# Kernel tuning notes

Measured on AMD Instinct MI355X. Metric: run time of the kernel, lower is better.

## Reference

```python
import jax, jax.numpy as jnp
import numpy as np

HID = 64  # GRU hidden size fixed in source: layers.GRU(64, ...)


def setup_inputs() -> dict:
    key = jax.random.key(0)
    ks = jax.random.split(key, 9)
    B, T, D, K = 128, 1024, 128, 32
    s = 0.05
    X = jax.random.normal(ks[0], (B, T, D), jnp.float32)
    mask = jnp.ones((B, T), jnp.int32)  # 1 = valid token
    # Keras GRU (reset_after=True) params
    gru_kernel = jax.random.normal(ks[1], (D, 3 * HID), jnp.float32) * s
    gru_rec_kernel = jax.random.normal(ks[2], (HID, 3 * HID), jnp.float32) * s
    gru_bias = jax.random.normal(ks[3], (2, 3 * HID), jnp.float32) * s  # [input_bias, recurrent_bias]
    # tfa.layers.CRF params: dense projection + chain kernel + boundary energies
    dense_kernel = jax.random.normal(ks[4], (HID, K), jnp.float32) * s
    dense_bias = jax.random.normal(ks[5], (K,), jnp.float32) * s
    chain_kernel = jax.random.normal(ks[6], (K, K), jnp.float32) * s
    left_boundary = jax.random.normal(ks[7], (K,), jnp.float32) * s
    right_boundary = jax.random.normal(ks[8], (K,), jnp.float32) * s
    return {"X": X, "mask": mask, "gru_kernel": gru_kernel,
            "gru_rec_kernel": gru_rec_kernel, "gru_bias": gru_bias,
            "dense_kernel": dense_kernel, "dense_bias": dense_bias,
            "chain_kernel": chain_kernel, "left_boundary": left_boundary,
            "right_boundary": right_boundary}


def gru_forward(X, mask_bool, gru_kernel, gru_rec_kernel, gru_bias):
    # Keras GRU, reset_after=True: z/r/h gate ordering, tanh/sigmoid activations.
    B, T, D = X.shape
    xproj = X @ gru_kernel + gru_bias[0]  # [B,T,3H] input projection (fused GEMM)

    def step(h, inp):
        xp, mt = inp  # xp: [B,3H], mt: [B] bool
        rec = h @ gru_rec_kernel + gru_bias[1]  # [B,3H]
        xz, xr, xh = jnp.split(xp, 3, axis=-1)
        rz, rr, rh = jnp.split(rec, 3, axis=-1)
        z = jax.nn.sigmoid(xz + rz)
        r = jax.nn.sigmoid(xr + rr)
        hh = jnp.tanh(xh + r * rh)
        hn = z * h + (1.0 - z) * hh
        hn = jnp.where(mt[:, None], hn, h)  # masked steps carry state
        return hn, hn

    h0 = jnp.zeros((B, HID), X.dtype)
    _, hs = jax.lax.scan(step, h0, (jnp.swapaxes(xproj, 0, 1), jnp.swapaxes(mask_bool, 0, 1)))
    return jnp.swapaxes(hs, 0, 1)  # [B,T,H]


def viterbi_decode(potentials, chain_kernel):
    # Max-plus DP with backpointers; potentials: [B,T,K]
    pots = jnp.swapaxes(potentials, 0, 1)  # [T,B,K]

    def fwd(score, pot_t):
        s = score[:, :, None] + chain_kernel[None]  # [B,K_from,K_to]
        bp = jnp.argmax(s, axis=1).astype(jnp.int32)  # [B,K]
        new_score = jnp.max(s, axis=1) + pot_t
        return new_score, bp

    final_score, bps = jax.lax.scan(fwd, pots[0], pots[1:])  # bps: [T-1,B,K]
    last_tag = jnp.argmax(final_score, axis=-1).astype(jnp.int32)  # [B]

    def back(tag, bp):
        prev = jnp.take_along_axis(bp, tag[:, None], axis=1)[:, 0]
        return prev, tag

    first_tag, tags = jax.lax.scan(back, last_tag, bps, reverse=True)  # tags[t] = tag at step t+1
    decoded = jnp.concatenate([first_tag[None], tags], axis=0)  # [T,B]
    return jnp.swapaxes(decoded, 0, 1)  # [B,T]


def reference(X, mask, gru_kernel, gru_rec_kernel, gru_bias,
              dense_kernel, dense_bias, chain_kernel,
              left_boundary, right_boundary):
    B, T, D = X.shape
    mask_bool = mask == 1
    hidden = gru_forward(X, mask_bool, gru_kernel, gru_rec_kernel, gru_bias)
    potentials = hidden @ dense_kernel + dense_bias  # [B,T,K] emissions
    seq_len = jnp.sum(mask, axis=1).astype(jnp.int32)  # [B]
    # Boundary energies (tfa CRF use_boundary=True): left at t=0, right at last valid step
    potentials = potentials.at[:, 0].add(left_boundary)
    potentials = potentials.at[jnp.arange(B), seq_len - 1].add(right_boundary)
    decoded = viterbi_decode(potentials, chain_kernel)  # [B,T] int32
    return decoded, potentials, seq_len, chain_kernel
```

## Files before the change

### kernel.cpp

```cpp
#include <hip/hip_runtime.h>
#include <math.h>

#define BB 128
#define TT 1024
#define DD 128
#define HH 64
#define G3 192
#define KK 32
#define CH 32

__global__ __launch_bounds__(256, 2) void xproj_kernel(const float* __restrict__ X,
                                                       const float* __restrict__ Wk,
                                                       const float* __restrict__ gbias,
                                                       float* __restrict__ xp) {
    __shared__ float Xs[64 * 132];
    __shared__ float Ws[128 * 68];
    const int tid = threadIdx.x;
    const int row0 = blockIdx.x * 64;
    const int cg = blockIdx.y;
#pragma unroll
    for (int it = 0; it < 8; ++it) {
        int idx = it * 1024 + tid * 4;
        int r = idx >> 7, c = idx & 127;
        float4 v = *(const float4*)&X[((size_t)(row0 + r)) * DD + c];
        *(float4*)&Xs[r * 132 + c] = v;
    }
#pragma unroll
    for (int it = 0; it < 8; ++it) {
        int idx = it * 1024 + tid * 4;
        int k = idx >> 6, c = idx & 63;
        float4 v = *(const float4*)&Wk[(size_t)k * G3 + cg * 64 + c];
        *(float4*)&Ws[k * 68 + c] = v;
    }
    __syncthreads();
    const int tr = tid >> 4, tc = tid & 15;
    const int r0 = tr * 4, c0 = tc * 4;
    float acc[4][4];
#pragma unroll
    for (int r = 0; r < 4; ++r)
#pragma unroll
        for (int c = 0; c < 4; ++c) acc[r][c] = 0.f;
#pragma unroll 4
    for (int k = 0; k < DD; k += 4) {
        float a[4][4];
#pragma unroll
        for (int r = 0; r < 4; ++r) {
            float4 t = *(const float4*)&Xs[(r0 + r) * 132 + k];
            a[r][0] = t.x; a[r][1] = t.y; a[r][2] = t.z; a[r][3] = t.w;
        }
#pragma unroll
        for (int kk = 0; kk < 4; ++kk) {
            float4 b = *(const float4*)&Ws[(k + kk) * 68 + c0];
#pragma unroll
            for (int r = 0; r < 4; ++r) {
                acc[r][0] += a[r][kk] * b.x;
                acc[r][1] += a[r][kk] * b.y;
                acc[r][2] += a[r][kk] * b.z;
                acc[r][3] += a[r][kk] * b.w;
            }
        }
    }
    float4 bias = *(const float4*)&gbias[cg * 64 + c0];
#pragma unroll
    for (int r = 0; r < 4; ++r) {
        float4 o;
        o.x = acc[r][0] + bias.x; o.y = acc[r][1] + bias.y;
        o.z = acc[r][2] + bias.z; o.w = acc[r][3] + bias.w;
        *(float4*)&xp[((size_t)(row0 + r0 + r)) * G3 + cg * 64 + c0] = o;
    }
}

#define BCAST(v, l) __int_as_float(__builtin_amdgcn_readlane(__float_as_int(v), (l)))

__global__ __launch_bounds__(320, 1)
void fused_kernel(const float* __restrict__ xp,
                  const float* __restrict__ Wr,
                  const float* __restrict__ gbias,
                  const int* __restrict__ mask,
                  const float* __restrict__ Dk,
                  const float* __restrict__ db,
                  const float* __restrict__ chain,
                  const float* __restrict__ lb,
                  const float* __restrict__ rb,
                  float* __restrict__ out_pot,
                  float* __restrict__ out_dec,
                  float* __restrict__ out_slen,
                  float* __restrict__ out_chn) {
    const int b = blockIdx.x;
    const int tid = threadIdx.x;
    const int w = tid >> 6;
    const int l = tid & 63;
    const int bTT = b * TT;

    __shared__ unsigned char bp[(TT - 1) * KK];
    __shared__ unsigned char table[32 * 32 * KK];
    __shared__ int ent[32];
    __shared__ int last_tag_s;
    __shared__ float gbuf[2][4 * HH];
    __shared__ __align__(16) float hbuf[4][HH];
    __shared__ __align__(16) float potring[64][KK];
    __shared__ __align__(16) float xpstage[2][CH * G3];
    __shared__ int maskst[2][CH];

    if (w < 3) {
        const int j = l;
        float wg[HH];
#pragma unroll
        for (int i2 = 0; i2 < HH; ++i2) wg[i2] = Wr[i2 * G3 + w * HH + j];
#pragma unroll
        for (int i2 = 0; i2 < HH; ++i2) asm volatile("" : "+v"(wg[i2]));
        const float bw = gbias[G3 + w * HH + j];
        __builtin_amdgcn_s_setprio(1);
        float h = 0.f;
        __syncthreads();
        float xv0 = xpstage[0][tid];
        int m0 = maskst[0][0];
        for (int i = 0; i < TT + 2; ++i) {
            if (i < TT) {
                float a0 = bw, a1 = 0.f, a2 = 0.f, a3 = 0.f;
#pragma unroll
                for (int c = 0; c < HH; c += 4) {
                    a0 += BCAST(h, c + 0) * wg[c + 0];
                    a1 += BCAST(h, c + 1) * wg[c + 1];
                    a2 += BCAST(h, c + 2) * wg[c + 2];
                    a3 += BCAST(h, c + 3) * wg[c + 3];
                }
                float a = (a0 + a1) + (a2 + a3);
                float g = (w == 2) ? a : 1.f / (1.f + __expf(-(xv0 + a)));
                gbuf[i & 1][w * HH + j] = g;
                if (w == 2) gbuf[i & 1][3 * HH + j] = xv0;
            }
            __syncthreads();
            if (i < TT) {
                float z  = gbuf[i & 1][j];
                float r  = gbuf[i & 1][HH + j];
                float rh = gbuf[i & 1][2 * HH + j];
                float xh = gbuf[i & 1][3 * HH + j];
                float y = xh + r * rh;
                float hh = 1.f - 2.f / (1.f + __expf(2.f * y));
                float hn = z * h + (1.f - z) * hh;
                hn = (m0 != 0) ? hn : h;
                h = hn;
                if (w == 0) hbuf[i & 3][j] = hn;
                if (i < TT - 1) {
                    const int t1 = i + 1;
                    xv0 = xpstage[(t1 >> 5) & 1][(t1 & 31) * G3 + tid];
                    m0  = maskst[(t1 >> 5) & 1][t1 & 31];
                }
            }
        }
    } else if (w == 3) {
        const int k = l & 31;
        int sl = 0;
#pragma unroll
        for (int q = 0; q < 16; ++q) sl += mask[bTT + q * 64 + l];
#pragma unroll
        for (int d = 32; d >= 1; d >>= 1) sl += __shfl_xor(sl, d, 64);
        if (l == 0) out_slen[b] = (float)sl;
        float dk[HH];
#pragma unroll
        for (int i2 = 0; i2 < HH; ++i2) dk[i2] = Dk[i2 * KK + k];
#pragma unroll
        for (int i2 = 0; i2 < HH; ++i2) asm volatile("" : "+v"(dk[i2]));
        const float dbk = db[k], lbk = lb[k], rbk = rb[k];
        const float* xpg = xp + (size_t)bTT * G3;
        float* potg = out_pot + (size_t)bTT * KK;
#pragma unroll
        for (int q = 0; q < 24; ++q) {
            float4 v = *(const float4*)&xpg[q * 256 + l * 4];
            *(float4*)&xpstage[0][q * 256 + l * 4] = v;
        }
        if (l < CH) maskst[0][l] = mask[bTT + l];
        __syncthreads();
        for (int i = 0; i < TT + 2; ++i) {
            if ((i & 31) == 0) {
                const int cn = (i >> 5) + 1;
                if (cn < 32) {
                    const float* src = xpg + (size_t)cn * CH * G3;
                    float* dst = &xpstage[cn & 1][0];
#pragma unroll
                    for (int q = 0; q < 24; ++q) {
                        float4 v = *(const float4*)&src[q * 256 + l * 4];
                        *(float4*)&dst[q * 256 + l * 4] = v;
                    }
                    if (l < CH) maskst[cn & 1][l] = mask[bTT + cn * CH + l];
                }
                const int cf = (i >> 5) - 2;
                if (cf >= 0) {
                    const float* srcl = &potring[(cf & 1) * 32][0];
                    float* dstg = potg + (size_t)cf * CH * KK;
#pragma unroll
                    for (int q = 0; q < 4; ++q) {
                        float4 v = *(const float4*)&srcl[q * 256 + l * 4];
                        *(float4*)&dstg[q * 256 + l * 4] = v;
                    }
                }
            }
            const int t = i - 2;
            if (t >= 0 && t < TT) {
                const float4* hv4 = (const float4*)&hbuf[t & 3][0];
                float p0 = dbk, p1 = 0.f, p2 = 0.f, p3 = 0.f;
#pragma unroll
                for (int c = 0; c < 16; ++c) {
                    float4 hv = hv4[c];
                    p0 += hv.x * dk[4 * c + 0];
                    p1 += hv.y * dk[4 * c + 1];
                    p2 += hv.z * dk[4 * c + 2];
                    p3 += hv.w * dk[4 * c + 3];
                }
                float pot = (p0 + p1) + (p2 + p3);
                if (t == 0) pot += lbk;
                if (t == sl - 1) pot += rbk;
                if (l < 32) potring[t & 63][k] = pot;
            }
            __syncthreads();
        }
        {
            const float* srcl = &potring[(31 & 1) * 32][0];
            float* dstg = potg + (size_t)31 * CH * KK;
#pragma unroll
            for (int q = 0; q < 4; ++q) {
                float4 v = *(const float4*)&srcl[q * 256 + l * 4];
                *(float4*)&dstg[q * 256 + l * 4] = v;
            }
        }
    } else {
        const int k = l & 31;
        const int hf = l >> 5;
        float ccol[16];
        int addr[16];
#pragma unroll
        for (int m = 0; m < 16; ++m) {
            ccol[m] = chain[(hf * 16 + m) * KK + k];
            addr[m] = (hf * 16 + m) * 4;
        }
#pragma unroll
        for (int m = 0; m < 16; ++m) asm volatile("" : "+v"(ccol[m]));
        const int addrx = (l ^ 32) * 4;
        float s = 0.f;
        __syncthreads();
        for (int i = 0; i < TT + 2; ++i) {
            __syncthreads();
            const int t = i - 2;
            if (t >= 0 && t < TT) {
                float pot = potring[t & 63][k];
                if (t == 0) {
                    s = pot;
                } else {
                    const int si = __float_as_int(s);
                    float c[16];
#pragma unroll
                    for (int m = 0; m < 16; ++m)
                        c[m] = __int_as_float(__builtin_amdgcn_ds_bpermute(addr[m], si)) + ccol[m];
                    float v1[8]; int i1[8];
#pragma unroll
                    for (int p = 0; p < 8; ++p) {
                        bool tk = c[2 * p + 1] > c[2 * p];
                        v1[p] = tk ? c[2 * p + 1] : c[2 * p];
                        i1[p] = hf * 16 + (tk ? 2 * p + 1 : 2 * p);
                    }
                    float v2[4]; int i2[4];
#pragma unroll
                    for (int p = 0; p < 4; ++p) {
                        bool tk = v1[2 * p + 1] > v1[2 * p];
                        v2[p] = tk ? v1[2 * p + 1] : v1[2 * p];
                        i2[p] = tk ? i1[2 * p + 1] : i1[2 * p];
                    }
                    float v3[2]; int i3[2];
#pragma unroll
                    for (int p = 0; p < 2; ++p) {
                        bool tk = v2[2 * p + 1] > v2[2 * p];
                        v3[p] = tk ? v2[2 * p + 1] : v2[2 * p];
                        i3[p] = tk ? i2[2 * p + 1] : i2[2 * p];
                    }
                    bool tk = v3[1] > v3[0];
                    float bv = tk ? v3[1] : v3[0];
                    int bi = tk ? i3[1] : i3[0];
                    float ov = __int_as_float(__builtin_amdgcn_ds_bpermute(addrx, __float_as_int(bv)));
                    int   oi = __builtin_amdgcn_ds_bpermute(addrx, bi);
                    bool take = (ov > bv) || (ov == bv && oi < bi);
                    if (take) { bv = ov; bi = oi; }
                    if (l < 32) bp[(t - 1) * KK + k] = (unsigned char)bi;
                    s = bv + pot;
                }
            }
        }
        float bv = s; int bi = k;
#pragma unroll
        for (int d = 16; d >= 1; d >>= 1) {
            float ov = __shfl_xor(bv, d, 64);
            int   oi = __shfl_xor(bi, d, 64);
            bool take = (ov > bv) || (ov == bv && oi < bi);
            if (take) { bv = ov; bi = oi; }
        }
        if (l == 0) last_tag_s = bi;
    }
    __syncthreads();
    {
        const int k = tid & 31;
        const int grp = tid >> 5;
        for (int c = grp; c < 32; c += 10) {
            int tag = k;
            for (int ll = 31; ll >= 0; --ll) {
                const int t = c * 32 + ll;
                if (t < TT - 1) tag = bp[t * KK + tag];
                table[(c * 32 + ll) * KK + k] = (unsigned char)tag;
            }
        }
    }
    __syncthreads();
    if (tid == 0) {
        int e = last_tag_s;
        ent[31] = e;
        for (int c = 30; c >= 0; --c) { e = table[(c + 1) * 32 * KK + e]; ent[c] = e; }
    }
    __syncthreads();
    for (int t = tid; t < TT; t += 320) {
        const int c = t >> 5, ll = t & 31;
        out_dec[(size_t)bTT + t] = (float)table[(c * 32 + ll) * KK + ent[c]];
    }
    if (b == 0) {
        for (int i2 = tid; i2 < KK * KK; i2 += 320) out_chn[i2] = chain[i2];
    }
}

extern "C" void kernel_launch(void* const* d_in, const int* in_sizes, int n_in,
                              void* d_out, int out_size, void* d_ws, size_t ws_size,
                              hipStream_t stream) {
    const float* X     = (const float*)d_in[0];
    const int*   mask  = (const int*)d_in[1];
    const float* Wk    = (const float*)d_in[2];
    const float* Wr    = (const float*)d_in[3];
    const float* gb    = (const float*)d_in[4];
    const float* Dk    = (const float*)d_in[5];
    const float* db    = (const float*)d_in[6];
    const float* chain = (const float*)d_in[7];
    const float* lb    = (const float*)d_in[8];
    const float* rb    = (const float*)d_in[9];

    float* out = (float*)d_out;
    float* out_dec  = out;
    float* out_pot  = out + (size_t)BB * TT;
    float* out_slen = out + (size_t)BB * TT + (size_t)BB * TT * KK;
    float* out_chn  = out_slen + BB;

    float* xp = (float*)d_ws;

    xproj_kernel<<<dim3((BB * TT) / 64, 3), dim3(256), 0, stream>>>(X, Wk, gb, xp);
    fused_kernel<<<dim3(BB), dim3(320), 0, stream>>>(xp, Wr, gb, mask, Dk, db, chain,
                                                     lb, rb, out_pot, out_dec,
                                                     out_slen, out_chn);
}
```

Measured before the change: 898.2 us.

## Fuse GRU input projection into the recurrent kernel via producer warps

Drops the separate input-projection GEMM kernel and its workspace round trip. Three new wavefronts in the fused kernel compute the xproj chunks on the fly: each keeps a column of the input weights in registers and stages X through the backtrace table buffer, which is reused as scratch. The work is pipelined one chunk ahead of the recurrence with a per-step barrier. This removes a kernel launch and the global write and read of the projections, but raises the block to 512 threads and adds per-step work that the serial recurrence may have to wait on.

```diff
diff --git a/kernel.cpp b/kernel.cpp
--- a/kernel.cpp
+++ b/kernel.cpp
@@ -9,71 +9,11 @@
 #define KK 32
 #define CH 32
 
-__global__ __launch_bounds__(256, 2) void xproj_kernel(const float* __restrict__ X,
-                                                       const float* __restrict__ Wk,
-                                                       const float* __restrict__ gbias,
-                                                       float* __restrict__ xp) {
-    __shared__ float Xs[64 * 132];
-    __shared__ float Ws[128 * 68];
-    const int tid = threadIdx.x;
-    const int row0 = blockIdx.x * 64;
-    const int cg = blockIdx.y;
-#pragma unroll
-    for (int it = 0; it < 8; ++it) {
-        int idx = it * 1024 + tid * 4;
-        int r = idx >> 7, c = idx & 127;
-        float4 v = *(const float4*)&X[((size_t)(row0 + r)) * DD + c];
-        *(float4*)&Xs[r * 132 + c] = v;
-    }
-#pragma unroll
-    for (int it = 0; it < 8; ++it) {
-        int idx = it * 1024 + tid * 4;
-        int k = idx >> 6, c = idx & 63;
-        float4 v = *(const float4*)&Wk[(size_t)k * G3 + cg * 64 + c];
-        *(float4*)&Ws[k * 68 + c] = v;
-    }
-    __syncthreads();
-    const int tr = tid >> 4, tc = tid & 15;
-    const int r0 = tr * 4, c0 = tc * 4;
-    float acc[4][4];
-#pragma unroll
-    for (int r = 0; r < 4; ++r)
-#pragma unroll
-        for (int c = 0; c < 4; ++c) acc[r][c] = 0.f;
-#pragma unroll 4
-    for (int k = 0; k < DD; k += 4) {
-        float a[4][4];
-#pragma unroll
-        for (int r = 0; r < 4; ++r) {
-            float4 t = *(const float4*)&Xs[(r0 + r) * 132 + k];
-            a[r][0] = t.x; a[r][1] = t.y; a[r][2] = t.z; a[r][3] = t.w;
-        }
-#pragma unroll
-        for (int kk = 0; kk < 4; ++kk) {
-            float4 b = *(const float4*)&Ws[(k + kk) * 68 + c0];
-#pragma unroll
-            for (int r = 0; r < 4; ++r) {
-                acc[r][0] += a[r][kk] * b.x;
-                acc[r][1] += a[r][kk] * b.y;
-                acc[r][2] += a[r][kk] * b.z;
-                acc[r][3] += a[r][kk] * b.w;
-            }
-        }
-    }
-    float4 bias = *(const float4*)&gbias[cg * 64 + c0];
-#pragma unroll
-    for (int r = 0; r < 4; ++r) {
-        float4 o;
-        o.x = acc[r][0] + bias.x; o.y = acc[r][1] + bias.y;
-        o.z = acc[r][2] + bias.z; o.w = acc[r][3] + bias.w;
-        *(float4*)&xp[((size_t)(row0 + r0 + r)) * G3 + cg * 64 + c0] = o;
-    }
-}
-
 #define BCAST(v, l) __int_as_float(__builtin_amdgcn_readlane(__float_as_int(v), (l)))
 
-__global__ __launch_bounds__(320, 1)
-void fused_kernel(const float* __restrict__ xp,
+__global__ __launch_bounds__(512, 1)
+void fused_kernel(const float* __restrict__ X,
+                  const float* __restrict__ Wk,
                   const float* __restrict__ Wr,
                   const float* __restrict__ gbias,
                   const int* __restrict__ mask,
@@ -93,7 +33,7 @@
     const int bTT = b * TT;
 
     __shared__ unsigned char bp[(TT - 1) * KK];
-    __shared__ unsigned char table[32 * 32 * KK];
+    __shared__ __align__(16) unsigned char table[32 * 32 * KK];
     __shared__ int ent[32];
     __shared__ int last_tag_s;
     __shared__ float gbuf[2][4 * HH];
@@ -102,6 +42,9 @@
     __shared__ __align__(16) float xpstage[2][CH * G3];
     __shared__ int maskst[2][CH];
 
+    float* Xstage0 = (float*)&table[0];
+    float* Xstage1 = (float*)&table[CH * DD * 4];
+
     if (w < 3) {
         const int j = l;
         float wg[HH];
@@ -112,6 +55,7 @@
         const float bw = gbias[G3 + w * HH + j];
         __builtin_amdgcn_s_setprio(1);
         float h = 0.f;
+        __syncthreads();
         __syncthreads();
         float xv0 = xpstage[0][tid];
         int m0 = maskst[0][0];
@@ -163,28 +107,14 @@
 #pragma unroll
         for (int i2 = 0; i2 < HH; ++i2) asm volatile("" : "+v"(dk[i2]));
         const float dbk = db[k], lbk = lb[k], rbk = rb[k];
-        const float* xpg = xp + (size_t)bTT * G3;
         float* potg = out_pot + (size_t)bTT * KK;
-#pragma unroll
-        for (int q = 0; q < 24; ++q) {
-            float4 v = *(const float4*)&xpg[q * 256 + l * 4];
-            *(float4*)&xpstage[0][q * 256 + l * 4] = v;
-        }
         if (l < CH) maskst[0][l] = mask[bTT + l];
+        __syncthreads();
         __syncthreads();
         for (int i = 0; i < TT + 2; ++i) {
             if ((i & 31) == 0) {
                 const int cn = (i >> 5) + 1;
-                if (cn < 32) {
-                    const float* src = xpg + (size_t)cn * CH * G3;
-                    float* dst = &xpstage[cn & 1][0];
-#pragma unroll
-                    for (int q = 0; q < 24; ++q) {
-                        float4 v = *(const float4*)&src[q * 256 + l * 4];
-                        *(float4*)&dst[q * 256 + l * 4] = v;
-                    }
-                    if (l < CH) maskst[cn & 1][l] = mask[bTT + cn * CH + l];
-                }
+                if (cn < 32 && l < CH) maskst[cn & 1][l] = mask[bTT + cn * CH + l];
                 const int cf = (i >> 5) - 2;
                 if (cf >= 0) {
                     const float* srcl = &potring[(cf & 1) * 32][0];
@@ -224,6 +154,81 @@
                 *(float4*)&dstg[q * 256 + l * 4] = v;
             }
         }
+    } else if (w < 7) {
+        const int xw = w - 4;
+        const int col = xw * 64 + l;
+        float wk[DD];
+#pragma unroll
+        for (int k2 = 0; k2 < DD; ++k2) wk[k2] = Wk[(size_t)k2 * G3 + col];
+#pragma unroll
+        for (int k2 = 0; k2 < DD; ++k2) asm volatile("" : "+v"(wk[k2]));
+        const float b0 = gbias[col];
+        const float* Xg = X + (size_t)bTT * DD;
+        {
+            const float* src0 = Xg;
+            const float* src1 = Xg + (size_t)CH * DD;
+#pragma unroll
+            for (int q = 0; q < 6; ++q) {
+                int idx = q * 192 + col;
+                if (idx < 1024) {
+                    float4 v0 = *(const float4*)&src0[idx * 4];
+                    *(float4*)&Xstage0[idx * 4] = v0;
+                    float4 v1 = *(const float4*)&src1[idx * 4];
+                    *(float4*)&Xstage1[idx * 4] = v1;
+                }
+            }
+        }
+        __syncthreads();
+#pragma unroll 1
+        for (int r = 0; r < CH; ++r) {
+            const float4* xr = (const float4*)&Xstage0[r * DD];
+            float acc = 0.f;
+#pragma unroll 4
+            for (int c4 = 0; c4 < 32; ++c4) {
+                float4 xv = xr[c4];
+                acc += xv.x * wk[4 * c4 + 0];
+                acc += xv.y * wk[4 * c4 + 1];
+                acc += xv.z * wk[4 * c4 + 2];
+                acc += xv.w * wk[4 * c4 + 3];
+            }
+            xpstage[0][r * G3 + col] = acc + b0;
+        }
+        __syncthreads();
+        for (int i = 0; i < TT + 2; ++i) {
+            const int wi = i >> 5;
+            if ((i & 31) == 0) {
+                const int cs = wi + 2;
+                if (cs < 32) {
+                    const float* src = Xg + (size_t)cs * CH * DD;
+                    float* dst = (cs & 1) ? Xstage1 : Xstage0;
+#pragma unroll
+                    for (int q = 0; q < 6; ++q) {
+                        int idx = q * 192 + col;
+                        if (idx < 1024) {
+                            float4 v = *(const float4*)&src[idx * 4];
+                            *(float4*)&dst[idx * 4] = v;
+                        }
+                    }
+                }
+            }
+            const int c = wi + 1;
+            if (c < 32) {
+                const int r = i & 31;
+                const float* xsrc = (c & 1) ? Xstage1 : Xstage0;
+                const float4* xr = (const float4*)&xsrc[r * DD];
+                float acc = 0.f;
+#pragma unroll 4
+                for (int c4 = 0; c4 < 32; ++c4) {
+                    float4 xv = xr[c4];
+                    acc += xv.x * wk[4 * c4 + 0];
+                    acc += xv.y * wk[4 * c4 + 1];
+                    acc += xv.z * wk[4 * c4 + 2];
+                    acc += xv.w * wk[4 * c4 + 3];
+                }
+                xpstage[c & 1][r * G3 + col] = acc + b0;
+            }
+            __syncthreads();
+        }
     } else {
         const int k = l & 31;
         const int hf = l >> 5;
@@ -238,6 +243,7 @@
         for (int m = 0; m < 16; ++m) asm volatile("" : "+v"(ccol[m]));
         const int addrx = (l ^ 32) * 4;
         float s = 0.f;
+        __syncthreads();
         __syncthreads();
         for (int i = 0; i < TT + 2; ++i) {
             __syncthreads();
@@ -299,7 +305,7 @@
     {
         const int k = tid & 31;
         const int grp = tid >> 5;
-        for (int c = grp; c < 32; c += 10) {
+        for (int c = grp; c < 32; c += 16) {
             int tag = k;
             for (int ll = 31; ll >= 0; --ll) {
                 const int t = c * 32 + ll;
@@ -315,12 +321,12 @@
         for (int c = 30; c >= 0; --c) { e = table[(c + 1) * 32 * KK + e]; ent[c] = e; }
     }
     __syncthreads();
-    for (int t = tid; t < TT; t += 320) {
+    for (int t = tid; t < TT; t += 512) {
         const int c = t >> 5, ll = t & 31;
         out_dec[(size_t)bTT + t] = (float)table[(c * 32 + ll) * KK + ent[c]];
     }
     if (b == 0) {
-        for (int i2 = tid; i2 < KK * KK; i2 += 320) out_chn[i2] = chain[i2];
+        for (int i2 = tid; i2 < KK * KK; i2 += 512) out_chn[i2] = chain[i2];
     }
 }
 
@@ -344,10 +350,7 @@
     float* out_slen = out + (size_t)BB * TT + (size_t)BB * TT * KK;
     float* out_chn  = out_slen + BB;
 
-    float* xp = (float*)d_ws;
-
-    xproj_kernel<<<dim3((BB * TT) / 64, 3), dim3(256), 0, stream>>>(X, Wk, gb, xp);
-    fused_kernel<<<dim3(BB), dim3(320), 0, stream>>>(xp, Wr, gb, mask, Dk, db, chain,
-                                                     lb, rb, out_pot, out_dec,
+    fused_kernel<<<dim3(BB), dim3(512), 0, stream>>>(X, Wk, Wr, gb, mask, Dk, db,
+                                                     chain, lb, rb, out_pot, out_dec,
                                                      out_slen, out_chn);
 }
```

After: 3.111 ms. 246% more time.

## Merge input projection and recurrent kernel into one launch with per-chunk flag handoff

Applied to the files above, without the earlier changes.

Replaces the separate projection GEMM launch with a single kernel of 2*BB blocks. The first BB blocks compute each sequence's input projection in 64-row tiles and raise global flags as tiles finish. The remaining BB blocks run the GRU/CRF recurrence and spin on those flags before staging each chunk, so the projection overlaps the serial recurrence instead of running before it. The cost is one block per sequence doing the GEMM, which is less parallel than the old grid, and the scheme depends on producer blocks being co-resident with the spinning consumers to avoid deadlock.

```diff
diff --git a/kernel.cpp b/kernel.cpp
--- a/kernel.cpp
+++ b/kernel.cpp
@@ -9,98 +9,112 @@
 #define KK 32
 #define CH 32
 
-__global__ __launch_bounds__(256, 2) void xproj_kernel(const float* __restrict__ X,
-                                                       const float* __restrict__ Wk,
-                                                       const float* __restrict__ gbias,
-                                                       float* __restrict__ xp) {
-    __shared__ float Xs[64 * 132];
-    __shared__ float Ws[128 * 68];
+#define BCAST(v, l) __int_as_float(__builtin_amdgcn_readlane(__float_as_int(v), (l)))
+
+__device__ int g_flags[BB * 32];
+
+__global__ __launch_bounds__(320, 1)
+void mega_kernel(const float* __restrict__ X,
+                 const float* __restrict__ Wk,
+                 const float* __restrict__ Wr,
+                 const float* __restrict__ gbias,
+                 const int* __restrict__ mask,
+                 const float* __restrict__ Dk,
+                 const float* __restrict__ db,
+                 const float* __restrict__ chain,
+                 const float* __restrict__ lb,
+                 const float* __restrict__ rb,
+                 float* __restrict__ xp,
+                 float* __restrict__ out_pot,
+                 float* __restrict__ out_dec,
+                 float* __restrict__ out_slen,
+                 float* __restrict__ out_chn) {
+    __shared__ __align__(16) unsigned char smem[138240];
     const int tid = threadIdx.x;
-    const int row0 = blockIdx.x * 64;
-    const int cg = blockIdx.y;
-#pragma unroll
-    for (int it = 0; it < 8; ++it) {
-        int idx = it * 1024 + tid * 4;
-        int r = idx >> 7, c = idx & 127;
-        float4 v = *(const float4*)&X[((size_t)(row0 + r)) * DD + c];
-        *(float4*)&Xs[r * 132 + c] = v;
-    }
-#pragma unroll
-    for (int it = 0; it < 8; ++it) {
-        int idx = it * 1024 + tid * 4;
-        int k = idx >> 6, c = idx & 63;
-        float4 v = *(const float4*)&Wk[(size_t)k * G3 + cg * 64 + c];
-        *(float4*)&Ws[k * 68 + c] = v;
-    }
-    __syncthreads();
-    const int tr = tid >> 4, tc = tid & 15;
-    const int r0 = tr * 4, c0 = tc * 4;
-    float acc[4][4];
-#pragma unroll
-    for (int r = 0; r < 4; ++r)
-#pragma unroll
-        for (int c = 0; c < 4; ++c) acc[r][c] = 0.f;
+
+    if (blockIdx.x < BB) {
+        const int p = blockIdx.x;
+        const int bTT = p * TT;
+        float* Xs = (float*)smem;
+        float* Ws = (float*)(smem + 33792);
+        for (int idx = tid; idx < 6144; idx += 320) {
+            const int cg = idx >> 11, rem = idx & 2047;
+            const int k = rem >> 4, c4 = (rem & 15) << 2;
+            float4 v = *(const float4*)&Wk[(size_t)k * G3 + cg * 64 + c4];
+            *(float4*)&Ws[cg * (128 * 68) + k * 68 + c4] = v;
+        }
+        const int tr = tid >> 4, tc = tid & 15;
+        const int r0 = tr * 4, c0 = tc * 4;
+        for (int rt = 0; rt < 16; ++rt) {
+            const int row0 = rt * 64;
+            for (int idx = tid; idx < 2048; idx += 320) {
+                const int r = idx >> 5, c4 = (idx & 31) << 2;
+                float4 v = *(const float4*)&X[((size_t)(bTT + row0 + r)) * DD + c4];
+                *(float4*)&Xs[r * 132 + c4] = v;
+            }
+            __syncthreads();
+            if (tid < 256) {
+                for (int cg = 0; cg < 3; ++cg) {
+                    const float* Wc = &Ws[cg * (128 * 68)];
+                    float acc[4][4];
+#pragma unroll
+                    for (int r = 0; r < 4; ++r)
+#pragma unroll
+                        for (int c = 0; c < 4; ++c) acc[r][c] = 0.f;
 #pragma unroll 4
-    for (int k = 0; k < DD; k += 4) {
-        float a[4][4];
-#pragma unroll
-        for (int r = 0; r < 4; ++r) {
-            float4 t = *(const float4*)&Xs[(r0 + r) * 132 + k];
-            a[r][0] = t.x; a[r][1] = t.y; a[r][2] = t.z; a[r][3] = t.w;
-        }
-#pragma unroll
-        for (int kk = 0; kk < 4; ++kk) {
-            float4 b = *(const float4*)&Ws[(k + kk) * 68 + c0];
-#pragma unroll
-            for (int r = 0; r < 4; ++r) {
-                acc[r][0] += a[r][kk] * b.x;
-                acc[r][1] += a[r][kk] * b.y;
-                acc[r][2] += a[r][kk] * b.z;
-                acc[r][3] += a[r][kk] * b.w;
-            }
-        }
-    }
-    float4 bias = *(const float4*)&gbias[cg * 64 + c0];
-#pragma unroll
-    for (int r = 0; r < 4; ++r) {
-        float4 o;
-        o.x = acc[r][0] + bias.x; o.y = acc[r][1] + bias.y;
-        o.z = acc[r][2] + bias.z; o.w = acc[r][3] + bias.w;
-        *(float4*)&xp[((size_t)(row0 + r0 + r)) * G3 + cg * 64 + c0] = o;
-    }
-}
-
-#define BCAST(v, l) __int_as_float(__builtin_amdgcn_readlane(__float_as_int(v), (l)))
-
-__global__ __launch_bounds__(320, 1)
-void fused_kernel(const float* __restrict__ xp,
-                  const float* __restrict__ Wr,
-                  const float* __restrict__ gbias,
-                  const int* __restrict__ mask,
-                  const float* __restrict__ Dk,
-                  const float* __restrict__ db,
-                  const float* __restrict__ chain,
-                  const float* __restrict__ lb,
-                  const float* __restrict__ rb,
-                  float* __restrict__ out_pot,
-                  float* __restrict__ out_dec,
-                  float* __restrict__ out_slen,
-                  float* __restrict__ out_chn) {
-    const int b = blockIdx.x;
-    const int tid = threadIdx.x;
+                    for (int k = 0; k < DD; k += 4) {
+                        float a[4][4];
+#pragma unroll
+                        for (int r = 0; r < 4; ++r) {
+                            float4 t = *(const float4*)&Xs[(r0 + r) * 132 + k];
+                            a[r][0] = t.x; a[r][1] = t.y; a[r][2] = t.z; a[r][3] = t.w;
+                        }
+#pragma unroll
+                        for (int kk = 0; kk < 4; ++kk) {
+                            float4 bv = *(const float4*)&Wc[(k + kk) * 68 + c0];
+#pragma unroll
+                            for (int r = 0; r < 4; ++r) {
+                                acc[r][0] += a[r][kk] * bv.x;
+                                acc[r][1] += a[r][kk] * bv.y;
+                                acc[r][2] += a[r][kk] * bv.z;
+                                acc[r][3] += a[r][kk] * bv.w;
+                            }
+                        }
+                    }
+                    float4 bias = *(const float4*)&gbias[cg * 64 + c0];
+#pragma unroll
+                    for (int r = 0; r < 4; ++r) {
+                        float4 o;
+                        o.x = acc[r][0] + bias.x; o.y = acc[r][1] + bias.y;
+                        o.z = acc[r][2] + bias.z; o.w = acc[r][3] + bias.w;
+                        *(float4*)&xp[((size_t)(bTT + row0 + r0 + r)) * G3 + cg * 64 + c0] = o;
+                    }
+                }
+            }
+            __threadfence();
+            __syncthreads();
+            if (tid == 0) {
+                atomicExch(&g_flags[p * 32 + 2 * rt], 1);
+                atomicExch(&g_flags[p * 32 + 2 * rt + 1], 1);
+            }
+        }
+        return;
+    }
+
+    const int b = blockIdx.x - BB;
     const int w = tid >> 6;
     const int l = tid & 63;
     const int bTT = b * TT;
 
-    __shared__ unsigned char bp[(TT - 1) * KK];
-    __shared__ unsigned char table[32 * 32 * KK];
-    __shared__ int ent[32];
-    __shared__ int last_tag_s;
-    __shared__ float gbuf[2][4 * HH];
-    __shared__ __align__(16) float hbuf[4][HH];
-    __shared__ __align__(16) float potring[64][KK];
-    __shared__ __align__(16) float xpstage[2][CH * G3];
-    __shared__ int maskst[2][CH];
+    unsigned char* bp    = smem;
+    unsigned char* table = smem + 32736;
+    int*   ent        = (int*)(smem + 65504);
+    int*   last_tag_s = (int*)(smem + 65632);
+    float (*gbuf)[4 * HH]   = (float (*)[4 * HH])(smem + 65648);
+    float (*hbuf)[HH]       = (float (*)[HH])(smem + 67696);
+    float (*potring)[KK]    = (float (*)[KK])(smem + 68720);
+    float (*xpstage)[CH * G3] = (float (*)[CH * G3])(smem + 76912);
+    int (*maskst)[CH]       = (int (*)[CH])(smem + 126064);
 
     if (w < 3) {
         const int j = l;
@@ -165,6 +179,10 @@
         const float dbk = db[k], lbk = lb[k], rbk = rb[k];
         const float* xpg = xp + (size_t)bTT * G3;
         float* potg = out_pot + (size_t)bTT * KK;
+        if (l == 0) {
+            while (atomicAdd(&g_flags[b * 32], 0) == 0) __builtin_amdgcn_s_sleep(8);
+        }
+        __threadfence();
 #pragma unroll
         for (int q = 0; q < 24; ++q) {
             float4 v = *(const float4*)&xpg[q * 256 + l * 4];
@@ -176,6 +194,11 @@
             if ((i & 31) == 0) {
                 const int cn = (i >> 5) + 1;
                 if (cn < 32) {
+                    if (l == 0) {
+                        while (atomicAdd(&g_flags[b * 32 + cn], 0) == 0)
+                            __builtin_amdgcn_s_sleep(8);
+                    }
+                    __threadfence();
                     const float* src = xpg + (size_t)cn * CH * G3;
                     float* dst = &xpstage[cn & 1][0];
 #pragma unroll
@@ -293,7 +316,7 @@
             bool take = (ov > bv) || (ov == bv && oi < bi);
             if (take) { bv = ov; bi = oi; }
         }
-        if (l == 0) last_tag_s = bi;
+        if (l == 0) *last_tag_s = bi;
     }
     __syncthreads();
     {
@@ -310,7 +333,7 @@
     }
     __syncthreads();
     if (tid == 0) {
-        int e = last_tag_s;
+        int e = *last_tag_s;
         ent[31] = e;
         for (int c = 30; c >= 0; --c) { e = table[(c + 1) * 32 * KK + e]; ent[c] = e; }
     }
@@ -319,9 +342,10 @@
         const int c = t >> 5, ll = t & 31;
         out_dec[(size_t)bTT + t] = (float)table[(c * 32 + ll) * KK + ent[c]];
     }
-    if (b == 0) {
+    if (blockIdx.x == BB) {
         for (int i2 = tid; i2 < KK * KK; i2 += 320) out_chn[i2] = chain[i2];
     }
+    for (int i2 = tid; i2 < 32; i2 += 320) atomicExch(&g_flags[b * 32 + i2], 0);
 }
 
 extern "C" void kernel_launch(void* const* d_in, const int* in_sizes, int n_in,
@@ -346,8 +370,7 @@
 
     float* xp = (float*)d_ws;
 
-    xproj_kernel<<<dim3((BB * TT) / 64, 3), dim3(256), 0, stream>>>(X, Wk, gb, xp);
-    fused_kernel<<<dim3(BB), dim3(320), 0, stream>>>(xp, Wr, gb, mask, Dk, db, chain,
-                                                     lb, rb, out_pot, out_dec,
-                                                     out_slen, out_chn);
+    mega_kernel<<<dim3(2 * BB), dim3(320), 0, stream>>>(X, Wk, Wr, gb, mask, Dk, db,
+                                                        chain, lb, rb, xp, out_pot,
+                                                        out_dec, out_slen, out_chn);
 }
```

Measured after the change: 926.0 us. 1.03x slower.

## Split GRU and Viterbi into separate blocks linked by global flags

Applied to the files above, without the earlier changes.

The recurrence now runs in a single wave per batch row: that wave computes all three gates plus the emission projection, holding the z weights and dense kernel in registers and reading the r/h weights from LDS, so the per-step block-wide barrier disappears. Viterbi moves to a second set of blocks that poll per-chunk global flags and stream potentials from global memory into a double buffer in LDS. The aim is to shorten the serial per-timestep critical path by removing the cross-wave syncs. The cost is more work per step in one wave, extra LDS weight loads, and reliance on producer and consumer blocks being co-resident, which risks deadlock if the Viterbi blocks are scheduled before their GRU blocks.

```diff
diff --git a/kernel.cpp b/kernel.cpp
--- a/kernel.cpp
+++ b/kernel.cpp
@@ -8,6 +8,10 @@
 #define G3 192
 #define KK 32
 #define CH 32
+
+#define BCAST(v, l) __int_as_float(__builtin_amdgcn_readlane(__float_as_int(v), (l)))
+
+__device__ int g_pflags[BB * 32];
 
 __global__ __launch_bounds__(256, 2) void xproj_kernel(const float* __restrict__ X,
                                                        const float* __restrict__ Wk,
@@ -70,165 +74,141 @@
     }
 }
 
-#define BCAST(v, l) __int_as_float(__builtin_amdgcn_readlane(__float_as_int(v), (l)))
-
-__global__ __launch_bounds__(320, 1)
-void fused_kernel(const float* __restrict__ xp,
-                  const float* __restrict__ Wr,
-                  const float* __restrict__ gbias,
-                  const int* __restrict__ mask,
-                  const float* __restrict__ Dk,
-                  const float* __restrict__ db,
-                  const float* __restrict__ chain,
-                  const float* __restrict__ lb,
-                  const float* __restrict__ rb,
-                  float* __restrict__ out_pot,
-                  float* __restrict__ out_dec,
-                  float* __restrict__ out_slen,
-                  float* __restrict__ out_chn) {
-    const int b = blockIdx.x;
+__global__ __launch_bounds__(256, 1)
+void gruvit_kernel(const float* __restrict__ xp,
+                   const float* __restrict__ Wr,
+                   const float* __restrict__ gbias,
+                   const int* __restrict__ mask,
+                   const float* __restrict__ Dk,
+                   const float* __restrict__ db,
+                   const float* __restrict__ chain,
+                   const float* __restrict__ lb,
+                   const float* __restrict__ rb,
+                   float* __restrict__ out_pot,
+                   float* __restrict__ out_dec,
+                   float* __restrict__ out_slen,
+                   float* __restrict__ out_chn) {
     const int tid = threadIdx.x;
     const int w = tid >> 6;
     const int l = tid & 63;
-    const int bTT = b * TT;
-
+
+    __shared__ __align__(16) float wl[2][16][64][4];
     __shared__ unsigned char bp[(TT - 1) * KK];
-    __shared__ unsigned char table[32 * 32 * KK];
+    __shared__ __align__(16) unsigned char table[32 * 32 * KK];
+    __shared__ __align__(16) float potbuf[2][CH][KK];
     __shared__ int ent[32];
     __shared__ int last_tag_s;
-    __shared__ float gbuf[2][4 * HH];
-    __shared__ __align__(16) float hbuf[4][HH];
-    __shared__ __align__(16) float potring[64][KK];
-    __shared__ __align__(16) float xpstage[2][CH * G3];
-    __shared__ int maskst[2][CH];
-
-    if (w < 3) {
+
+    if (blockIdx.x < BB) {
+        if (w != 0) return;
+        const int b = blockIdx.x;
+        const int bTT = b * TT;
         const int j = l;
-        float wg[HH];
-#pragma unroll
-        for (int i2 = 0; i2 < HH; ++i2) wg[i2] = Wr[i2 * G3 + w * HH + j];
-#pragma unroll
-        for (int i2 = 0; i2 < HH; ++i2) asm volatile("" : "+v"(wg[i2]));
-        const float bw = gbias[G3 + w * HH + j];
-        __builtin_amdgcn_s_setprio(1);
-        float h = 0.f;
-        __syncthreads();
-        float xv0 = xpstage[0][tid];
-        int m0 = maskst[0][0];
-        for (int i = 0; i < TT + 2; ++i) {
-            if (i < TT) {
-                float a0 = bw, a1 = 0.f, a2 = 0.f, a3 = 0.f;
-#pragma unroll
-                for (int c = 0; c < HH; c += 4) {
-                    a0 += BCAST(h, c + 0) * wg[c + 0];
-                    a1 += BCAST(h, c + 1) * wg[c + 1];
-                    a2 += BCAST(h, c + 2) * wg[c + 2];
-                    a3 += BCAST(h, c + 3) * wg[c + 3];
-                }
-                float a = (a0 + a1) + (a2 + a3);
-                float g = (w == 2) ? a : 1.f / (1.f + __expf(-(xv0 + a)));
-                gbuf[i & 1][w * HH + j] = g;
-                if (w == 2) gbuf[i & 1][3 * HH + j] = xv0;
-            }
-            __syncthreads();
-            if (i < TT) {
-                float z  = gbuf[i & 1][j];
-                float r  = gbuf[i & 1][HH + j];
-                float rh = gbuf[i & 1][2 * HH + j];
-                float xh = gbuf[i & 1][3 * HH + j];
-                float y = xh + r * rh;
-                float hh = 1.f - 2.f / (1.f + __expf(2.f * y));
-                float hn = z * h + (1.f - z) * hh;
-                hn = (m0 != 0) ? hn : h;
-                h = hn;
-                if (w == 0) hbuf[i & 3][j] = hn;
-                if (i < TT - 1) {
-                    const int t1 = i + 1;
-                    xv0 = xpstage[(t1 >> 5) & 1][(t1 & 31) * G3 + tid];
-                    m0  = maskst[(t1 >> 5) & 1][t1 & 31];
-                }
-            }
-        }
-    } else if (w == 3) {
         const int k = l & 31;
+        for (int g = 0; g < 2; ++g)
+            for (int c4 = 0; c4 < 16; ++c4)
+                for (int e = 0; e < 4; ++e)
+                    wl[g][c4][j][e] = Wr[(size_t)(4 * c4 + e) * G3 + 64 + g * 64 + j];
+        float wgz[64];
+#pragma unroll
+        for (int c = 0; c < 64; ++c) wgz[c] = Wr[(size_t)c * G3 + j];
+#pragma unroll
+        for (int c = 0; c < 64; ++c) asm volatile("" : "+v"(wgz[c]));
+        float dk[64];
+#pragma unroll
+        for (int c = 0; c < 64; ++c) dk[c] = Dk[c * KK + k];
+#pragma unroll
+        for (int c = 0; c < 64; ++c) asm volatile("" : "+v"(dk[c]));
+        const float bwz = gbias[G3 + j], bwr = gbias[G3 + 64 + j], bwh = gbias[G3 + 128 + j];
+        const float dbk = db[k], lbk = lb[k], rbk = rb[k];
         int sl = 0;
 #pragma unroll
         for (int q = 0; q < 16; ++q) sl += mask[bTT + q * 64 + l];
 #pragma unroll
         for (int d = 32; d >= 1; d >>= 1) sl += __shfl_xor(sl, d, 64);
         if (l == 0) out_slen[b] = (float)sl;
-        float dk[HH];
-#pragma unroll
-        for (int i2 = 0; i2 < HH; ++i2) dk[i2] = Dk[i2 * KK + k];
-#pragma unroll
-        for (int i2 = 0; i2 < HH; ++i2) asm volatile("" : "+v"(dk[i2]));
-        const float dbk = db[k], lbk = lb[k], rbk = rb[k];
         const float* xpg = xp + (size_t)bTT * G3;
         float* potg = out_pot + (size_t)bTT * KK;
-#pragma unroll
-        for (int q = 0; q < 24; ++q) {
-            float4 v = *(const float4*)&xpg[q * 256 + l * 4];
-            *(float4*)&xpstage[0][q * 256 + l * 4] = v;
-        }
-        if (l < CH) maskst[0][l] = mask[bTT + l];
-        __syncthreads();
-        for (int i = 0; i < TT + 2; ++i) {
-            if ((i & 31) == 0) {
-                const int cn = (i >> 5) + 1;
-                if (cn < 32) {
-                    const float* src = xpg + (size_t)cn * CH * G3;
-                    float* dst = &xpstage[cn & 1][0];
-#pragma unroll
-                    for (int q = 0; q < 24; ++q) {
-                        float4 v = *(const float4*)&src[q * 256 + l * 4];
-                        *(float4*)&dst[q * 256 + l * 4] = v;
-                    }
-                    if (l < CH) maskst[cn & 1][l] = mask[bTT + cn * CH + l];
-                }
-                const int cf = (i >> 5) - 2;
-                if (cf >= 0) {
-                    const float* srcl = &potring[(cf & 1) * 32][0];
-                    float* dstg = potg + (size_t)cf * CH * KK;
-#pragma unroll
-                    for (int q = 0; q < 4; ++q) {
-                        float4 v = *(const float4*)&srcl[q * 256 + l * 4];
-                        *(float4*)&dstg[q * 256 + l * 4] = v;
+        float h = 0.f;
+        float xz = xpg[j], xr = xpg[64 + j], xh = xpg[128 + j];
+        int m0 = mask[bTT];
+        for (int t = 0; t < TT; ++t) {
+            float nxz = 0.f, nxr = 0.f, nxh = 0.f; int nm = 0;
+            if (t + 1 < TT) {
+                const float* p1 = xpg + (size_t)(t + 1) * G3;
+                nxz = p1[j]; nxr = p1[64 + j]; nxh = p1[128 + j];
+                nm = mask[bTT + t + 1];
+            }
+            float az0 = bwz, az1 = 0.f, az2 = 0.f, az3 = 0.f;
+            float ar0 = bwr, ar1 = 0.f, ar2 = 0.f, ar3 = 0.f;
+            float ah0 = bwh, ah1 = 0.f, ah2 = 0.f, ah3 = 0.f;
+            float p0 = dbk, p1a = 0.f, p2a = 0.f, p3a = 0.f;
+#pragma unroll
+            for (int c4 = 0; c4 < 16; ++c4) {
+                float4 wr4 = *(const float4*)&wl[0][c4][j][0];
+                float4 wh4 = *(const float4*)&wl[1][c4][j][0];
+                float h0 = BCAST(h, 4 * c4 + 0), h1 = BCAST(h, 4 * c4 + 1);
+                float h2 = BCAST(h, 4 * c4 + 2), h3 = BCAST(h, 4 * c4 + 3);
+                az0 += h0 * wgz[4 * c4 + 0]; az1 += h1 * wgz[4 * c4 + 1];
+                az2 += h2 * wgz[4 * c4 + 2]; az3 += h3 * wgz[4 * c4 + 3];
+                ar0 += h0 * wr4.x; ar1 += h1 * wr4.y; ar2 += h2 * wr4.z; ar3 += h3 * wr4.w;
+                ah0 += h0 * wh4.x; ah1 += h1 * wh4.y; ah2 += h2 * wh4.z; ah3 += h3 * wh4.w;
+                p0 += h0 * dk[4 * c4 + 0]; p1a += h1 * dk[4 * c4 + 1];
+                p2a += h2 * dk[4 * c4 + 2]; p3a += h3 * dk[4 * c4 + 3];
+            }
+            if (t > 0) {
+                const int tp = t - 1;
+                float pot = (p0 + p1a) + (p2a + p3a);
+                if (tp == 0) pot += lbk;
+                if (tp == sl - 1) pot += rbk;
+                if (l < 32) potg[(size_t)tp * KK + k] = pot;
+                if ((t & 31) == 0) {
+                    if (l == 0) {
+                        __threadfence();
+                        atomicExch(&g_pflags[b * 32 + ((t - 1) >> 5)], 1);
                     }
                 }
             }
-            const int t = i - 2;
-            if (t >= 0 && t < TT) {
-                const float4* hv4 = (const float4*)&hbuf[t & 3][0];
-                float p0 = dbk, p1 = 0.f, p2 = 0.f, p3 = 0.f;
-#pragma unroll
-                for (int c = 0; c < 16; ++c) {
-                    float4 hv = hv4[c];
-                    p0 += hv.x * dk[4 * c + 0];
-                    p1 += hv.y * dk[4 * c + 1];
-                    p2 += hv.z * dk[4 * c + 2];
-                    p3 += hv.w * dk[4 * c + 3];
-                }
-                float pot = (p0 + p1) + (p2 + p3);
-                if (t == 0) pot += lbk;
-                if (t == sl - 1) pot += rbk;
-                if (l < 32) potring[t & 63][k] = pot;
-            }
-            __syncthreads();
+            float az = (az0 + az1) + (az2 + az3);
+            float ar = (ar0 + ar1) + (ar2 + ar3);
+            float ah = (ah0 + ah1) + (ah2 + ah3);
+            float z = 1.f / (1.f + __expf(-(xz + az)));
+            float r = 1.f / (1.f + __expf(-(xr + ar)));
+            float y = xh + r * ah;
+            float hh = 1.f - 2.f / (1.f + __expf(2.f * y));
+            float hn = z * h + (1.f - z) * hh;
+            h = (m0 != 0) ? hn : h;
+            xz = nxz; xr = nxr; xh = nxh; m0 = nm;
         }
         {
-            const float* srcl = &potring[(31 & 1) * 32][0];
-            float* dstg = potg + (size_t)31 * CH * KK;
-#pragma unroll
-            for (int q = 0; q < 4; ++q) {
-                float4 v = *(const float4*)&srcl[q * 256 + l * 4];
-                *(float4*)&dstg[q * 256 + l * 4] = v;
-            }
-        }
-    } else {
-        const int k = l & 31;
-        const int hf = l >> 5;
-        float ccol[16];
-        int addr[16];
+            float p0 = dbk, p1a = 0.f, p2a = 0.f, p3a = 0.f;
+#pragma unroll
+            for (int c4 = 0; c4 < 16; ++c4) {
+                p0  += BCAST(h, 4 * c4 + 0) * dk[4 * c4 + 0];
+                p1a += BCAST(h, 4 * c4 + 1) * dk[4 * c4 + 1];
+                p2a += BCAST(h, 4 * c4 + 2) * dk[4 * c4 + 2];
+                p3a += BCAST(h, 4 * c4 + 3) * dk[4 * c4 + 3];
+            }
+            float pot = (p0 + p1a) + (p2a + p3a);
+            if (TT - 1 == sl - 1) pot += rbk;
+            if (l < 32) potg[(size_t)(TT - 1) * KK + k] = pot;
+            if (l == 0) {
+                __threadfence();
+                atomicExch(&g_pflags[b * 32 + 31], 1);
+            }
+        }
+        return;
+    }
+
+    const int b = blockIdx.x - BB;
+    const int bTT = b * TT;
+    const float* potg = out_pot + (size_t)bTT * KK;
+    const int k = l & 31;
+    const int hf = l >> 5;
+    const int addrx = (l ^ 32) * 4;
+    float ccol[16];
+    int addr[16];
+    if (w == 1) {
 #pragma unroll
         for (int m = 0; m < 16; ++m) {
             ccol[m] = chain[(hf * 16 + m) * KK + k];
@@ -236,27 +216,51 @@
         }
 #pragma unroll
         for (int m = 0; m < 16; ++m) asm volatile("" : "+v"(ccol[m]));
-        const int addrx = (l ^ 32) * 4;
-        float s = 0.f;
-        __syncthreads();
-        for (int i = 0; i < TT + 2; ++i) {
-            __syncthreads();
-            const int t = i - 2;
-            if (t >= 0 && t < TT) {
-                float pot = potring[t & 63][k];
+    }
+    if (w == 0) {
+        if (l == 0) {
+            while (atomicAdd(&g_pflags[b * 32 + 0], 0) == 0) __builtin_amdgcn_s_sleep(8);
+        }
+        __threadfence();
+#pragma unroll
+        for (int q = 0; q < 4; ++q) {
+            float4 v = *(const float4*)&potg[(size_t)(q * 64 + l) * 4];
+            ((float4*)&potbuf[0][0][0])[q * 64 + l] = v;
+        }
+    }
+    __syncthreads();
+    float s = 0.f;
+    for (int c = 0; c < 32; ++c) {
+        if (w == 0 && c + 1 < 32) {
+            if (l == 0) {
+                while (atomicAdd(&g_pflags[b * 32 + c + 1], 0) == 0)
+                    __builtin_amdgcn_s_sleep(8);
+            }
+            __threadfence();
+            const float* src = potg + (size_t)(c + 1) * CH * KK;
+#pragma unroll
+            for (int q = 0; q < 4; ++q) {
+                float4 v = *(const float4*)&src[(size_t)(q * 64 + l) * 4];
+                ((float4*)&potbuf[(c + 1) & 1][0][0])[q * 64 + l] = v;
+            }
+        }
+        if (w == 1) {
+            for (int ll = 0; ll < 32; ++ll) {
+                const int t = c * 32 + ll;
+                float pot = potbuf[c & 1][ll][k];
                 if (t == 0) {
                     s = pot;
                 } else {
                     const int si = __float_as_int(s);
-                    float c[16];
+                    float cc[16];
 #pragma unroll
                     for (int m = 0; m < 16; ++m)
-                        c[m] = __int_as_float(__builtin_amdgcn_ds_bpermute(addr[m], si)) + ccol[m];
+                        cc[m] = __int_as_float(__builtin_amdgcn_ds_bpermute(addr[m], si)) + ccol[m];
                     float v1[8]; int i1[8];
 #pragma unroll
                     for (int p = 0; p < 8; ++p) {
-                        bool tk = c[2 * p + 1] > c[2 * p];
-                        v1[p] = tk ? c[2 * p + 1] : c[2 * p];
+                        bool tk = cc[2 * p + 1] > cc[2 * p];
+                        v1[p] = tk ? cc[2 * p + 1] : cc[2 * p];
                         i1[p] = hf * 16 + (tk ? 2 * p + 1 : 2 * p);
                     }
                     float v2[4]; int i2[4];
@@ -285,6 +289,9 @@
                 }
             }
         }
+        __syncthreads();
+    }
+    if (w == 1) {
         float bv = s; int bi = k;
 #pragma unroll
         for (int d = 16; d >= 1; d >>= 1) {
@@ -297,14 +304,14 @@
     }
     __syncthreads();
     {
-        const int k = tid & 31;
+        const int kk2 = tid & 31;
         const int grp = tid >> 5;
-        for (int c = grp; c < 32; c += 10) {
-            int tag = k;
+        for (int c = grp; c < 32; c += 8) {
+            int tag = kk2;
             for (int ll = 31; ll >= 0; --ll) {
                 const int t = c * 32 + ll;
                 if (t < TT - 1) tag = bp[t * KK + tag];
-                table[(c * 32 + ll) * KK + k] = (unsigned char)tag;
+                table[(c * 32 + ll) * KK + kk2] = (unsigned char)tag;
             }
         }
     }
@@ -315,13 +322,14 @@
         for (int c = 30; c >= 0; --c) { e = table[(c + 1) * 32 * KK + e]; ent[c] = e; }
     }
     __syncthreads();
-    for (int t = tid; t < TT; t += 320) {
+    for (int t = tid; t < TT; t += 256) {
         const int c = t >> 5, ll = t & 31;
         out_dec[(size_t)bTT + t] = (float)table[(c * 32 + ll) * KK + ent[c]];
     }
-    if (b == 0) {
-        for (int i2 = tid; i2 < KK * KK; i2 += 320) out_chn[i2] = chain[i2];
-    }
+    if (blockIdx.x == BB) {
+        for (int i2 = tid; i2 < KK * KK; i2 += 256) out_chn[i2] = chain[i2];
+    }
+    for (int i2 = tid; i2 < 32; i2 += 256) atomicExch(&g_pflags[b * 32 + i2], 0);
 }
 
 extern "C" void kernel_launch(void* const* d_in, const int* in_sizes, int n_in,
@@ -347,7 +355,7 @@
     float* xp = (float*)d_ws;
 
     xproj_kernel<<<dim3((BB * TT) / 64, 3), dim3(256), 0, stream>>>(X, Wk, gb, xp);
-    fused_kernel<<<dim3(BB), dim3(320), 0, stream>>>(xp, Wr, gb, mask, Dk, db, chain,
-                                                     lb, rb, out_pot, out_dec,
-                                                     out_slen, out_chn);
+    gruvit_kernel<<<dim3(2 * BB), dim3(256), 0, stream>>>(xp, Wr, gb, mask, Dk, db,
+                                                          chain, lb, rb, out_pot,
+                                                          out_dec, out_slen, out_chn);
 }
```

Result: slower. 1.144 ms (+27.4%).
